# Kernel tuning notes

Hardware: AMD Instinct MI355X
Metric: run time of the kernel (lower is better)

## Reference

```python
import jax, jax.numpy as jnp
import numpy as np

G, S, D, H, E = 8, 2048, 1024, 4096, 8  # groups, group_size, d_model, ffn_hidden, experts


def setup_inputs() -> dict:
    key = jax.random.key(0)
    ks = jax.random.split(key, 6)
    s = 0.02
    return {
        "x": jax.random.normal(ks[0], (G, S, D), dtype=jnp.float32),
        "gate_w": jax.random.normal(ks[1], (D, E), dtype=jnp.float32) * s,
        "ew1": jax.random.normal(ks[2], (E, D, H), dtype=jnp.float32) * s,
        "eb1": jnp.zeros((E, H), dtype=jnp.float32),
        "ew2": jax.random.normal(ks[3], (E, H, D), dtype=jnp.float32) * s,
        "eb2": jnp.zeros((E, D), dtype=jnp.float32),
        "sw1": jax.random.normal(ks[4], (D, H), dtype=jnp.float32) * s,
        "sb1": jnp.zeros((H,), dtype=jnp.float32),
        "sw2": jax.random.normal(ks[5], (H, D), dtype=jnp.float32) * s,
        "sb2": jnp.zeros((D,), dtype=jnp.float32),
        "expert_capacity": 2048,
    }


def reference(x, gate_w, ew1, eb1, ew2, eb2, sw1, sb1, sw2, sb2, expert_capacity):
    g, s_, d = x.shape
    e = gate_w.shape[1]
    T = g * s_
    cap = int(expert_capacity)

    # ---- Router (inference path) ----
    router_logits = jnp.einsum('gsd,de->gse', x, gate_w)           # (G,S,E)
    router_probs = jax.nn.softmax(router_logits, axis=-1)
    flat_probs = router_probs.transpose(2, 0, 1).reshape(e, T)      # (E,T)
    pad_w = max(0, cap - T)
    if pad_w > 0:
        flat_probs = jnp.pad(flat_probs, ((0, 0), (0, pad_w)),
                             mode='constant', constant_values=-1e9)
    scores, token_indices = jax.lax.top_k(flat_probs, k=cap)        # (E,C)
    scores = jnp.where(scores > -1e8, scores, 0.0)

    # ---- Routed experts: gather -> grouped FFN -> scale -> scatter-add ----
    x_flat = x.reshape(T, d)                                        # (T,D)
    safe_idx = jnp.clip(token_indices, 0, T - 1)                    # guard padded slots
    toks = x_flat[safe_idx]                                         # (E,C,D)
    h = jax.nn.gelu(jnp.einsum('ecd,edh->ech', toks, ew1) + eb1[:, None, :])
    y = jnp.einsum('ech,ehd->ecd', h, ew2) + eb2[:, None, :]        # (E,C,D)
    y = y * scores[..., None]                                       # zero weight kills padded slots
    routed = jnp.zeros_like(x_flat).at[safe_idx.reshape(-1)].add(y.reshape(-1, d))

    # ---- Shared expert over all tokens ----
    shared = jax.nn.gelu(x_flat @ sw1 + sb1) @ sw2 + sb2            # (T,D)

    return (routed + shared).reshape(g, s_, d)
```

## Files before the change

kernel.cpp:

```cpp
#include <hip/hip_runtime.h>

typedef __bf16 bf16;
typedef __bf16 bf16x8 __attribute__((ext_vector_type(8)));
typedef float f32x4 __attribute__((ext_vector_type(4)));

#define NTOK 16384
#define DMODEL 1024
#define HFFN 4096
#define NEXP 8
#define CAP 2048

#define VMCNT(n) asm volatile("s_waitcnt vmcnt(" #n ")" ::: "memory")
#define RAWBAR() do { __builtin_amdgcn_s_barrier(); __builtin_amdgcn_sched_barrier(0); } while (0)

__device__ __forceinline__ void gload16(const void* g, void* l) {
  __builtin_amdgcn_global_load_lds((const __attribute__((address_space(1))) void*)g,
                                   (__attribute__((address_space(3))) void*)l, 16, 0, 0);
}

__device__ __forceinline__ float gelu_f(float v) {
  float u = 0.7978845608028654f * (v + 0.044715f * v * v * v);
  float ex = __expf(2.0f * u);
  float th = 1.0f - 2.0f / (ex + 1.0f);
  return 0.5f * v * (1.0f + th);
}

__device__ __forceinline__ void xcd_remap(int& bx, int& by) {
  const int gx = gridDim.x;
  const int lg = 31 - __clz((unsigned)gx);
  const int w = blockIdx.x + gx * blockIdx.y;
  bx = (w >> 3) & (gx - 1);
  by = (w & 7) | (((w >> 3) >> lg) << 3);
}

__global__ __launch_bounds__(256) void cvt_x_kernel(const float* __restrict__ x,
                                                    bf16* __restrict__ xb) {
  int i = blockIdx.x * blockDim.x + threadIdx.x;
  const float4* a = (const float4*)x + (size_t)i * 2;
  float4 v0 = a[0], v1 = a[1];
  bf16x8 o;
  o[0]=(bf16)v0.x; o[1]=(bf16)v0.y; o[2]=(bf16)v0.z; o[3]=(bf16)v0.w;
  o[4]=(bf16)v1.x; o[5]=(bf16)v1.y; o[6]=(bf16)v1.z; o[7]=(bf16)v1.w;
  *(bf16x8*)(xb + (size_t)i * 8) = o;
}

__global__ __launch_bounds__(64) void router_kernel(const float* __restrict__ x,
                                                    const float* __restrict__ gw,
                                                    float* __restrict__ probs) {
  int t = blockIdx.x;
  int l = threadIdx.x;
  int e = l & 7, chunk = l >> 3;
  const float* xr = x + (size_t)t * DMODEL + chunk * 128;
  const float* gwr = gw + (size_t)(chunk * 128) * NEXP + e;
  float a0 = 0.f, a1 = 0.f;
  #pragma unroll
  for (int d = 0; d < 128; d += 8) {
    float4 xv = *(const float4*)(xr + d);
    float4 xw = *(const float4*)(xr + d + 4);
    a0 += xv.x * gwr[(d+0)*8] + xv.y * gwr[(d+1)*8] + xv.z * gwr[(d+2)*8] + xv.w * gwr[(d+3)*8];
    a1 += xw.x * gwr[(d+4)*8] + xw.y * gwr[(d+5)*8] + xw.z * gwr[(d+6)*8] + xw.w * gwr[(d+7)*8];
  }
  float acc = a0 + a1;
  acc += __shfl_xor(acc, 8);
  acc += __shfl_xor(acc, 16);
  acc += __shfl_xor(acc, 32);
  float m = acc;
  m = fmaxf(m, __shfl_xor(m, 1));
  m = fmaxf(m, __shfl_xor(m, 2));
  m = fmaxf(m, __shfl_xor(m, 4));
  float ex = expf(acc - m);
  float s = ex;
  s += __shfl_xor(s, 1); s += __shfl_xor(s, 2); s += __shfl_xor(s, 4);
  if (l < 8) probs[(size_t)e * NTOK + t] = ex / s;
}

__global__ __launch_bounds__(256) void topk_kernel(const float* __restrict__ probs,
                                                   int* __restrict__ oidx,
                                                   float* __restrict__ oscr) {
  const int e = blockIdx.x;
  const float* p = probs + (size_t)e * NTOK;
  const int t = threadIdx.x;
  __shared__ unsigned hist[256];
  __shared__ unsigned sg[256], sq[256];
  __shared__ unsigned bcast[4];
  unsigned pref = 0, krem = CAP;
  for (int pass = 0; pass < 4; ++pass) {
    const int sh = 24 - pass * 8;
    hist[t] = 0;
    __syncthreads();
    for (int j = 0; j < 64; ++j) {
      unsigned u = __float_as_uint(p[t * 64 + j]);
      bool ok = (pass == 0) || ((u >> (sh + 8)) == pref);
      if (ok) atomicAdd(&hist[(u >> sh) & 255u], 1u);
    }
    __syncthreads();
    if (t == 0) {
      unsigned cum = 0; int b = 255;
      for (; b > 0; --b) {
        unsigned c = hist[b];
        if (cum + c >= krem) break;
        cum += c;
      }
      bcast[0] = (pref << 8) | (unsigned)b;
      bcast[1] = krem - cum;
    }
    __syncthreads();
    pref = bcast[0];
    krem = bcast[1];
  }
  const unsigned thr = pref;
  const unsigned neq_take = krem;
  unsigned cgt = 0, ceq = 0;
  for (int j = 0; j < 64; ++j) {
    unsigned u = __float_as_uint(p[t * 64 + j]);
    cgt += (u > thr);
    ceq += (u == thr);
  }
  sg[t] = cgt; sq[t] = ceq;
  __syncthreads();
  if (t == 0) {
    unsigned ag = 0, aq = 0;
    for (int i = 0; i < 256; ++i) {
      unsigned g = sg[i], q = sq[i];
      sg[i] = ag; sq[i] = aq;
      ag += g; aq += q;
    }
    bcast[2] = ag;
  }
  __syncthreads();
  const unsigned ngt = bcast[2];
  unsigned og = sg[t], oq = sq[t];
  int* oi = oidx + e * CAP;
  float* os = oscr + e * CAP;
  for (int j = 0; j < 64; ++j) {
    int tok = t * 64 + j;
    float pv = p[tok];
    unsigned u = __float_as_uint(pv);
    if (u > thr) {
      oi[og] = tok; os[og] = pv; ++og;
    } else if (u == thr) {
      if (oq < neq_take) { oi[ngt + oq] = tok; os[ngt + oq] = pv; }
      ++oq;
    }
  }
}

__global__ __launch_bounds__(256) void transpose_cvt(const float* __restrict__ in_e,
                                                     const float* __restrict__ in_s,
                                                     bf16* __restrict__ outp,
                                                     int R, int C) {
  int z = blockIdx.z;
  const float* in = (z < 8) ? (in_e + (size_t)z * (size_t)R * C) : in_s;
  bf16* out = outp + (size_t)z * (size_t)R * C;
  __shared__ float tile[64][65];
  int tx = threadIdx.x & 63, ty = threadIdx.x >> 6;
  int c0 = blockIdx.x * 64, r0 = blockIdx.y * 64;
  #pragma unroll
  for (int j = 0; j < 16; ++j) {
    int r = ty + j * 4;
    tile[r][tx] = in[(size_t)(r0 + r) * C + c0 + tx];
  }
  __syncthreads();
  #pragma unroll
  for (int j = 0; j < 16; ++j) {
    int c = ty + j * 4;
    out[(size_t)(c0 + c) * R + r0 + tx] = (bf16)tile[tx][c];
  }
}


__global__ __launch_bounds__(512, 2) void ffn1_gemm(const bf16* __restrict__ xb,
                                                    const bf16* __restrict__ w1t,
                                                    const float* __restrict__ bias1,
                                                    const int* __restrict__ sel,
                                                    bf16* __restrict__ hout,
                                                    int routed) {
  const int e = blockIdx.z;
  const bf16* Bw = w1t + (routed ? (size_t)e * HFFN * DMODEL : 0);
  const float* bias = bias1 + (routed ? (size_t)e * HFFN : 0);
  bf16* hb = hout + (routed ? (size_t)e * CAP * HFFN : 0);
  int bx, by;
  xcd_remap(bx, by);
  const int m0 = by * 256, n0 = bx * 256;
  __shared__ __align__(16) bf16 smem[49152];
  const int tid = threadIdx.x, lane = tid & 63, wave = tid >> 6;
  const int wr = wave >> 2, wc = wave & 3;

  const int srow = tid >> 2, sch = tid & 3;
  const int schs = sch ^ ((srow >> 1) & 3);
  const int ldst = srow * 32 + sch * 8;
  const bf16 *srcA0, *srcA1, *srcB0, *srcB1;
  {
    int r0i = routed ? sel[e * CAP + m0 + srow] : (m0 + srow);
    int r1i = routed ? sel[e * CAP + m0 + 128 + srow] : (m0 + 128 + srow);
    srcA0 = xb + (size_t)r0i * DMODEL + schs * 8;
    srcA1 = xb + (size_t)r1i * DMODEL + schs * 8;
    srcB0 = Bw + (size_t)(n0 + srow) * DMODEL + schs * 8;
    srcB1 = Bw + (size_t)(n0 + 128 + srow) * DMODEL + schs * 8;
  }

  f32x4 acc[8][4];
  #pragma unroll
  for (int i = 0; i < 8; ++i)
    #pragma unroll
    for (int j = 0; j < 4; ++j) acc[i][j] = (f32x4){0.f, 0.f, 0.f, 0.f};

  const int fr = lane & 15;
  const int fch = ((lane >> 4) ^ ((lane >> 1) & 3)) * 8;
  const int NT = DMODEL / 32;

  #define STAGE1(t, b) do { \
    bf16* As_ = smem + (b) * 16384; \
    const int ko = (t) * 32; \
    gload16(srcA0 + ko, As_ + ldst); \
    gload16(srcA1 + ko, As_ + 4096 + ldst); \
    gload16(srcB0 + ko, As_ + 8192 + ldst); \
    gload16(srcB1 + ko, As_ + 12288 + ldst); \
  } while (0)

  STAGE1(0, 0);
  STAGE1(1, 1);
  VMCNT(4);
  RAWBAR();

  int b = 0;
  for (int t = 0; t < NT; ++t) {
    int b2 = b + 2; if (b2 >= 3) b2 -= 3;
    if (t + 2 < NT) STAGE1(t + 2, b2);
    const bf16* As = smem + b * 16384;
    const bf16* Bs = As + 8192;
    bf16x8 av[8], bv[4];
    #pragma unroll
    for (int i = 0; i < 8; ++i)
      av[i] = *(const bf16x8*)(As + (wr * 128 + i * 16 + fr) * 32 + fch);
    #pragma unroll
    for (int j = 0; j < 4; ++j)
      bv[j] = *(const bf16x8*)(Bs + (wc * 64 + j * 16 + fr) * 32 + fch);
    __builtin_amdgcn_s_setprio(1);
    #pragma unroll
    for (int i = 0; i < 8; ++i)
      #pragma unroll
      for (int j = 0; j < 4; ++j)
        acc[i][j] = __builtin_amdgcn_mfma_f32_16x16x32_bf16(av[i], bv[j], acc[i][j], 0, 0, 0);
    __builtin_amdgcn_s_setprio(0);
    if (t + 2 < NT) { VMCNT(4); } else { VMCNT(0); }
    RAWBAR();
    if (++b == 3) b = 0;
  }
  #undef STAGE1

  #pragma unroll
  for (int half = 0; half < 2; ++half) {
    if (wr == half) {
      #pragma unroll
      for (int i = 0; i < 8; ++i) {
        #pragma unroll
        for (int j = 0; j < 4; ++j) {
          const int nl = wc * 64 + j * 16 + fr;
          const float bb = bias[n0 + nl];
          #pragma unroll
          for (int q = 0; q < 4; ++q) {
            const int ml = i * 16 + (lane >> 4) * 4 + q;
            smem[ml * 256 + (nl ^ (((ml >> 2) & 7) << 4))] =
                (bf16)gelu_f(acc[i][j][q] + bb);
          }
        }
      }
    }
    __syncthreads();
    #pragma unroll
    for (int p = 0; p < 8; ++p) {
      const int flat = p * 512 + tid;
      const int row = flat >> 5, nc8 = flat & 31;
      uint4 v = *(const uint4*)(smem + row * 256 + ((nc8 * 8) ^ (((row >> 2) & 7) << 4)));
      *(uint4*)(hb + (size_t)(m0 + half * 128 + row) * HFFN + n0 + nc8 * 8) = v;
    }
    __syncthreads();
  }
}

__global__ __launch_bounds__(512, 2) void ffn2_gemm(const bf16* __restrict__ hbuf,
                                                    const bf16* __restrict__ w2t,
                                                    const float* __restrict__ bias2,
                                                    const int* __restrict__ sel,
                                                    const float* __restrict__ scr,
                                                    float* __restrict__ out,
                                                    int routed) {
  const int e = blockIdx.z;
  const bf16* Ab = hbuf + (routed ? (size_t)e * CAP * HFFN : 0);
  const bf16* Bw = w2t + (routed ? (size_t)e * DMODEL * HFFN : 0);
  const float* bias = bias2 + (routed ? (size_t)e * DMODEL : 0);
  int bx, by;
  xcd_remap(bx, by);
  const int m0 = by * 256, n0 = bx * 256;
  __shared__ __align__(16) bf16 smem[49152];
  __shared__ int s_tok[256];
  __shared__ float s_scl[256];
  const int tid = threadIdx.x, lane = tid & 63, wave = tid >> 6;
  const int wr = wave >> 2, wc = wave & 3;

  const int srow = tid >> 2, sch = tid & 3;
  const int schs = sch ^ ((srow >> 1) & 3);
  const int ldst = srow * 32 + sch * 8;
  const bf16* srcA0 = Ab + (size_t)(m0 + srow) * HFFN + schs * 8;
  const bf16* srcA1 = Ab + (size_t)(m0 + 128 + srow) * HFFN + schs * 8;
  const bf16* srcB0 = Bw + (size_t)(n0 + srow) * HFFN + schs * 8;
  const bf16* srcB1 = Bw + (size_t)(n0 + 128 + srow) * HFFN + schs * 8;
  if (routed && tid < 256) {
    s_tok[tid] = sel[e * CAP + m0 + tid];
    s_scl[tid] = scr[e * CAP + m0 + tid];
  }

  f32x4 acc[8][4];
  #pragma unroll
  for (int i = 0; i < 8; ++i)
    #pragma unroll
    for (int j = 0; j < 4; ++j) acc[i][j] = (f32x4){0.f, 0.f, 0.f, 0.f};

  const int fr = lane & 15;
  const int fch = ((lane >> 4) ^ ((lane >> 1) & 3)) * 8;
  const int NT = HFFN / 32;

  #define STAGE2(t, b) do { \
    bf16* As_ = smem + (b) * 16384; \
    const int ko = (t) * 32; \
    gload16(srcA0 + ko, As_ + ldst); \
    gload16(srcA1 + ko, As_ + 4096 + ldst); \
    gload16(srcB0 + ko, As_ + 8192 + ldst); \
    gload16(srcB1 + ko, As_ + 12288 + ldst); \
  } while (0)

  STAGE2(0, 0);
  STAGE2(1, 1);
  VMCNT(4);
  RAWBAR();

  int b = 0;
  for (int t = 0; t < NT; ++t) {
    int b2 = b + 2; if (b2 >= 3) b2 -= 3;
    if (t + 2 < NT) STAGE2(t + 2, b2);
    const bf16* As = smem + b * 16384;
    const bf16* Bs = As + 8192;
    bf16x8 av[8], bv[4];
    #pragma unroll
    for (int i = 0; i < 8; ++i)
      av[i] = *(const bf16x8*)(As + (wr * 128 + i * 16 + fr) * 32 + fch);
    #pragma unroll
    for (int j = 0; j < 4; ++j)
      bv[j] = *(const bf16x8*)(Bs + (wc * 64 + j * 16 + fr) * 32 + fch);
    __builtin_amdgcn_s_setprio(1);
    #pragma unroll
    for (int i = 0; i < 8; ++i)
      #pragma unroll
      for (int j = 0; j < 4; ++j)
        acc[i][j] = __builtin_amdgcn_mfma_f32_16x16x32_bf16(av[i], bv[j], acc[i][j], 0, 0, 0);
    __builtin_amdgcn_s_setprio(0);
    if (t + 2 < NT) { VMCNT(4); } else { VMCNT(0); }
    RAWBAR();
    if (++b == 3) b = 0;
  }
  #undef STAGE2

  if (!routed) {
    #pragma unroll
    for (int i = 0; i < 8; ++i) {
      #pragma unroll
      for (int j = 0; j < 4; ++j) {
        const int nl = wc * 64 + j * 16 + fr;
        const float bb = bias[n0 + nl];
        #pragma unroll
        for (int q = 0; q < 4; ++q) {
          const int ml = wr * 128 + i * 16 + (lane >> 4) * 4 + q;
          out[(size_t)(m0 + ml) * DMODEL + n0 + nl] = acc[i][j][q] + bb;
        }
      }
    }
  } else {
    __syncthreads();
    #pragma unroll
    for (int i = 0; i < 8; ++i) {
      #pragma unroll
      for (int j = 0; j < 4; ++j) {
        const int nl = wc * 64 + j * 16 + fr;
        const float bb = bias[n0 + nl];
        #pragma unroll
        for (int q = 0; q < 4; ++q) {
          const int ml = wr * 128 + i * 16 + (lane >> 4) * 4 + q;
          const int tok = s_tok[ml];
          const float sc = s_scl[ml];
          atomicAdd(out + (size_t)tok * DMODEL + n0 + nl, (acc[i][j][q] + bb) * sc);
        }
      }
    }
  }
}

extern "C" void kernel_launch(void* const* d_in, const int* in_sizes, int n_in,
                              void* d_out, int out_size, void* d_ws, size_t ws_size,
                              hipStream_t stream) {
  const float* x   = (const float*)d_in[0];
  const float* gw  = (const float*)d_in[1];
  const float* ew1 = (const float*)d_in[2];
  const float* eb1 = (const float*)d_in[3];
  const float* ew2 = (const float*)d_in[4];
  const float* eb2 = (const float*)d_in[5];
  const float* sw1 = (const float*)d_in[6];
  const float* sb1 = (const float*)d_in[7];
  const float* sw2 = (const float*)d_in[8];
  const float* sb2 = (const float*)d_in[9];
  float* out = (float*)d_out;

  char* ws = (char*)d_ws;
  size_t off = 0;
  bf16* xb      = (bf16*)(ws + off); off += (size_t)NTOK * DMODEL * 2;
  bf16* w1t     = (bf16*)(ws + off); off += (size_t)9 * HFFN * DMODEL * 2;
  bf16* w2t     = (bf16*)(ws + off); off += (size_t)9 * DMODEL * HFFN * 2;
  bf16* hbuf    = (bf16*)(ws + off); off += (size_t)NTOK * HFFN * 2;
  float* probs  = (float*)(ws + off); off += (size_t)NEXP * NTOK * 4;
  int* selidx   = (int*)(ws + off);   off += (size_t)NEXP * CAP * 4;
  float* selscr = (float*)(ws + off); off += (size_t)NEXP * CAP * 4;

  cvt_x_kernel<<<dim3(NTOK * DMODEL / 8 / 256), dim3(256), 0, stream>>>(x, xb);
  router_kernel<<<dim3(NTOK), dim3(64), 0, stream>>>(x, gw, probs);
  topk_kernel<<<dim3(NEXP), dim3(256), 0, stream>>>(probs, selidx, selscr);
  transpose_cvt<<<dim3(HFFN / 64, DMODEL / 64, 9), dim3(256), 0, stream>>>(ew1, sw1, w1t, DMODEL, HFFN);
  transpose_cvt<<<dim3(DMODEL / 64, HFFN / 64, 9), dim3(256), 0, stream>>>(ew2, sw2, w2t, HFFN, DMODEL);

  ffn1_gemm<<<dim3(HFFN / 256, NTOK / 256, 1), dim3(512), 0, stream>>>(
      xb, w1t + (size_t)8 * HFFN * DMODEL, sb1, (const int*)nullptr, hbuf, 0);
  ffn2_gemm<<<dim3(DMODEL / 256, NTOK / 256, 1), dim3(512), 0, stream>>>(
      hbuf, w2t + (size_t)8 * DMODEL * HFFN, sb2, (const int*)nullptr, (const float*)nullptr, out, 0);

  ffn1_gemm<<<dim3(HFFN / 256, CAP / 256, NEXP), dim3(512), 0, stream>>>(
      xb, w1t, eb1, selidx, hbuf, 1);
  ffn2_gemm<<<dim3(DMODEL / 256, CAP / 256, NEXP), dim3(512), 0, stream>>>(
      hbuf, w2t, eb2, selidx, selscr, out, 1);
}
```

Before: 991.3 us.

## Split GEMM k-step into four barrier-fenced MFMA phases interleaved with loads

Restructures the shared k-loop of both FFN GEMMs into four sub-phases. Each phase issues a subset of LDS fragment reads and one global->LDS load, then runs a 4x2 block of MFMAs, with explicit barriers and lgkmcnt waits between phases. The aim is to spread memory traffic across the MFMA stream and keep waves in lockstep, ping-pong style, so LDS reads and global loads overlap compute. The cost is many more barriers per k-step, which can stall waves if the phases are not balanced.

```diff
diff --git a/kernel.cpp b/kernel.cpp
--- a/kernel.cpp
+++ b/kernel.cpp
@@ -11,7 +11,11 @@
 #define CAP 2048
 
 #define VMCNT(n) asm volatile("s_waitcnt vmcnt(" #n ")" ::: "memory")
-#define RAWBAR() do { __builtin_amdgcn_s_barrier(); __builtin_amdgcn_sched_barrier(0); } while (0)
+#define LGKM0() do { asm volatile("s_waitcnt lgkmcnt(0)" ::: "memory"); \
+                     __builtin_amdgcn_sched_barrier(0); } while (0)
+#define RAWBAR() do { __builtin_amdgcn_sched_barrier(0); \
+                      __builtin_amdgcn_s_barrier(); \
+                      __builtin_amdgcn_sched_barrier(0); } while (0)
 
 __device__ __forceinline__ void gload16(const void* g, void* l) {
   __builtin_amdgcn_global_load_lds((const __attribute__((address_space(1))) void*)g,
@@ -168,6 +172,71 @@
   }
 }
 
+
+#define STAGE(t, bb) do { \
+  bf16* S_ = smem + (bb) * 16384; \
+  const int ko_ = (t) * 32; \
+  gload16(srcA0 + ko_, S_ + ldst); \
+  gload16(srcA1 + ko_, S_ + 4096 + ldst); \
+  gload16(srcB0 + ko_, S_ + 8192 + ldst); \
+  gload16(srcB1 + ko_, S_ + 12288 + ldst); \
+} while (0)
+
+#define MFMA_BLK(ILO, JLO) \
+  _Pragma("unroll") \
+  for (int i = 0; i < 4; ++i) \
+    _Pragma("unroll") \
+    for (int j = 0; j < 2; ++j) \
+      acc[(ILO) + i][(JLO) + j] = __builtin_amdgcn_mfma_f32_16x16x32_bf16( \
+          (ILO) ? avh[i] : avl[i], bv[(JLO) + j], acc[(ILO) + i][(JLO) + j], 0, 0, 0)
+
+#define KLOOP(NT) do { \
+  STAGE(0, 0); \
+  STAGE(1, 1); \
+  VMCNT(4); \
+  RAWBAR(); \
+  int b = 0; \
+  for (int t = 0; t < (NT); ++t) { \
+    int b2 = b + 2; if (b2 >= 3) b2 -= 3; \
+    const bool st = (t + 2 < (NT)); \
+    bf16* S2 = smem + b2 * 16384; \
+    const int ko2 = (t + 2) * 32; \
+    const bf16* As = smem + b * 16384; \
+    const bf16* Bs = As + 8192; \
+    bf16x8 avl[4], avh[4], bv[4]; \
+     \
+    _Pragma("unroll") \
+    for (int i = 0; i < 4; ++i) \
+      avl[i] = *(const bf16x8*)(As + (wr * 128 + i * 16 + fr) * 32 + fch); \
+    bv[0] = *(const bf16x8*)(Bs + (wc * 64 + fr) * 32 + fch); \
+    bv[1] = *(const bf16x8*)(Bs + (wc * 64 + 16 + fr) * 32 + fch); \
+    if (st) gload16(srcA0 + ko2, S2 + ldst); \
+    RAWBAR(); LGKM0(); \
+    __builtin_amdgcn_s_setprio(1); MFMA_BLK(0, 0); __builtin_amdgcn_s_setprio(0); \
+    RAWBAR(); \
+     \
+    bv[2] = *(const bf16x8*)(Bs + (wc * 64 + 32 + fr) * 32 + fch); \
+    bv[3] = *(const bf16x8*)(Bs + (wc * 64 + 48 + fr) * 32 + fch); \
+    if (st) gload16(srcA1 + ko2, S2 + 4096 + ldst); \
+    RAWBAR(); LGKM0(); \
+    __builtin_amdgcn_s_setprio(1); MFMA_BLK(0, 2); __builtin_amdgcn_s_setprio(0); \
+    RAWBAR(); \
+     \
+    _Pragma("unroll") \
+    for (int i = 0; i < 4; ++i) \
+      avh[i] = *(const bf16x8*)(As + (wr * 128 + 64 + i * 16 + fr) * 32 + fch); \
+    if (st) gload16(srcB0 + ko2, S2 + 8192 + ldst); \
+    RAWBAR(); LGKM0(); \
+    __builtin_amdgcn_s_setprio(1); MFMA_BLK(4, 0); __builtin_amdgcn_s_setprio(0); \
+    RAWBAR(); \
+     \
+    if (st) gload16(srcB1 + ko2, S2 + 12288 + ldst); \
+    __builtin_amdgcn_s_setprio(1); MFMA_BLK(4, 2); __builtin_amdgcn_s_setprio(0); \
+    if (st) { VMCNT(4); } else { VMCNT(0); } \
+    RAWBAR(); \
+    if (++b == 3) b = 0; \
+  } \
+} while (0)
 
 __global__ __launch_bounds__(512, 2) void ffn1_gemm(const bf16* __restrict__ xb,
                                                     const bf16* __restrict__ w1t,
@@ -207,47 +276,8 @@
 
   const int fr = lane & 15;
   const int fch = ((lane >> 4) ^ ((lane >> 1) & 3)) * 8;
-  const int NT = DMODEL / 32;
-
-  #define STAGE1(t, b) do { \
-    bf16* As_ = smem + (b) * 16384; \
-    const int ko = (t) * 32; \
-    gload16(srcA0 + ko, As_ + ldst); \
-    gload16(srcA1 + ko, As_ + 4096 + ldst); \
-    gload16(srcB0 + ko, As_ + 8192 + ldst); \
-    gload16(srcB1 + ko, As_ + 12288 + ldst); \
-  } while (0)
-
-  STAGE1(0, 0);
-  STAGE1(1, 1);
-  VMCNT(4);
-  RAWBAR();
-
-  int b = 0;
-  for (int t = 0; t < NT; ++t) {
-    int b2 = b + 2; if (b2 >= 3) b2 -= 3;
-    if (t + 2 < NT) STAGE1(t + 2, b2);
-    const bf16* As = smem + b * 16384;
-    const bf16* Bs = As + 8192;
-    bf16x8 av[8], bv[4];
-    #pragma unroll
-    for (int i = 0; i < 8; ++i)
-      av[i] = *(const bf16x8*)(As + (wr * 128 + i * 16 + fr) * 32 + fch);
-    #pragma unroll
-    for (int j = 0; j < 4; ++j)
-      bv[j] = *(const bf16x8*)(Bs + (wc * 64 + j * 16 + fr) * 32 + fch);
-    __builtin_amdgcn_s_setprio(1);
-    #pragma unroll
-    for (int i = 0; i < 8; ++i)
-      #pragma unroll
-      for (int j = 0; j < 4; ++j)
-        acc[i][j] = __builtin_amdgcn_mfma_f32_16x16x32_bf16(av[i], bv[j], acc[i][j], 0, 0, 0);
-    __builtin_amdgcn_s_setprio(0);
-    if (t + 2 < NT) { VMCNT(4); } else { VMCNT(0); }
-    RAWBAR();
-    if (++b == 3) b = 0;
-  }
-  #undef STAGE1
+
+  KLOOP(DMODEL / 32);
 
   #pragma unroll
   for (int half = 0; half < 2; ++half) {
@@ -319,47 +349,8 @@
 
   const int fr = lane & 15;
   const int fch = ((lane >> 4) ^ ((lane >> 1) & 3)) * 8;
-  const int NT = HFFN / 32;
-
-  #define STAGE2(t, b) do { \
-    bf16* As_ = smem + (b) * 16384; \
-    const int ko = (t) * 32; \
-    gload16(srcA0 + ko, As_ + ldst); \
-    gload16(srcA1 + ko, As_ + 4096 + ldst); \
-    gload16(srcB0 + ko, As_ + 8192 + ldst); \
-    gload16(srcB1 + ko, As_ + 12288 + ldst); \
-  } while (0)
-
-  STAGE2(0, 0);
-  STAGE2(1, 1);
-  VMCNT(4);
-  RAWBAR();
-
-  int b = 0;
-  for (int t = 0; t < NT; ++t) {
-    int b2 = b + 2; if (b2 >= 3) b2 -= 3;
-    if (t + 2 < NT) STAGE2(t + 2, b2);
-    const bf16* As = smem + b * 16384;
-    const bf16* Bs = As + 8192;
-    bf16x8 av[8], bv[4];
-    #pragma unroll
-    for (int i = 0; i < 8; ++i)
-      av[i] = *(const bf16x8*)(As + (wr * 128 + i * 16 + fr) * 32 + fch);
-    #pragma unroll
-    for (int j = 0; j < 4; ++j)
-      bv[j] = *(const bf16x8*)(Bs + (wc * 64 + j * 16 + fr) * 32 + fch);
-    __builtin_amdgcn_s_setprio(1);
-    #pragma unroll
-    for (int i = 0; i < 8; ++i)
-      #pragma unroll
-      for (int j = 0; j < 4; ++j)
-        acc[i][j] = __builtin_amdgcn_mfma_f32_16x16x32_bf16(av[i], bv[j], acc[i][j], 0, 0, 0);
-    __builtin_amdgcn_s_setprio(0);
-    if (t + 2 < NT) { VMCNT(4); } else { VMCNT(0); }
-    RAWBAR();
-    if (++b == 3) b = 0;
-  }
-  #undef STAGE2
+
+  KLOOP(HFFN / 32);
 
   if (!routed) {
     #pragma unroll
```

Result: no change. 976.8 us (-1.5%).
